# Kernel optimization log

Hardware: AMD Instinct MI355X
Metric: run time of the kernel (lower is better)

The kernel has to match this reference:

```python
import jax, jax.numpy as jnp
import numpy as np

B, T, C, K, NH, HID, L, NC = 16, 500, 512, 7, 8, 2048, 3, 2
HD = C // NH
SCALE = float(1.0 / np.sqrt(HD))


def setup_inputs() -> dict:
    key = jax.random.key(0)
    ks = jax.random.split(key, 24)
    rn = lambda k, sh, s=0.02: jax.random.normal(k, sh, jnp.float32) * s
    return {
        'x': jax.random.normal(ks[0], (B, T, C), jnp.float32),
        'dw_w': rn(ks[1], (L, NC, C, 1, K)),   # depthwise conv kernels (groups=C)
        'dw_b': rn(ks[2], (L, NC, C)),
        'pw_w': rn(ks[3], (L, NC, C, C)),       # pointwise 1x1 conv weights [out,in]
        'pw_b': rn(ks[4], (L, NC, C)),
        'cln_g': jnp.ones((L, NC, C), jnp.float32),
        'cln_b': jnp.zeros((L, NC, C), jnp.float32),
        'wq': rn(ks[5], (L, C, C)), 'bq': rn(ks[6], (L, C)),
        'wk': rn(ks[7], (L, C, C)), 'bk': rn(ks[8], (L, C)),
        'wv': rn(ks[9], (L, C, C)), 'bv': rn(ks[10], (L, C)),
        'wo': rn(ks[11], (L, C, C)), 'bo': rn(ks[12], (L, C)),
        'aln_g': jnp.ones((L, C), jnp.float32), 'aln_b': jnp.zeros((L, C), jnp.float32),
        'w1': rn(ks[13], (L, HID, C)), 'b1': rn(ks[14], (L, HID)),
        'w2': rn(ks[15], (L, C, HID)), 'b2': rn(ks[16], (L, C)),
        'fln_g': jnp.ones((L, C), jnp.float32), 'fln_b': jnp.zeros((L, C), jnp.float32),
    }


def _ln(x, g, b):
    m = x.mean(-1, keepdims=True)
    v = ((x - m) ** 2).mean(-1, keepdims=True)
    return (x - m) / jnp.sqrt(v + 1e-5) * g + b


def _conv_block(x, w, b, pw, pb, g, be):
    # x: (B, C, T). Depthwise conv (groups=C), padding K//2 keeps T.
    out = jax.lax.conv_general_dilated(
        x, w, window_strides=(1,), padding=[(K // 2, K // 2)],
        feature_group_count=C, dimension_numbers=('NCH', 'OIH', 'NCH')) + b[None, :, None]
    out = jnp.einsum('bct,oc->bot', out, pw) + pb[None, :, None]  # pointwise 1x1
    out = _ln(out.transpose(0, 2, 1), g, be).transpose(0, 2, 1)
    return out


def _attn(x, wq, bq, wk, bk, wv, bv, wo, bo):
    Bx, Tx, Cx = x.shape
    def split(h):
        return h.reshape(Bx, Tx, NH, HD).transpose(0, 2, 1, 3)  # (B,H,T,HD)
    q = split(x @ wq.T + bq)
    k = split(x @ wk.T + bk)
    v = split(x @ wv.T + bv)
    att = jnp.einsum('bhqd,bhkd->bhqk', q, k) * SCALE
    mask = jnp.tril(jnp.ones((Tx, Tx), bool))
    att = jnp.where(mask, att, -1e10)
    att = jax.nn.softmax(att, axis=-1)
    y = jnp.einsum('bhqk,bhkd->bhqd', att, v)
    y = y.transpose(0, 2, 1, 3).reshape(Bx, Tx, Cx)
    return y @ wo.T + bo


def _block(x, l, dw_w, dw_b, pw_w, pw_b, cln_g, cln_b, wq, bq, wk, bk, wv, bv,
           wo, bo, aln_g, aln_b, w1, b1, w2, b2, fln_g, fln_b):
    out = x.transpose(0, 2, 1)  # (B, C, T)
    for c in range(NC):
        out = _conv_block(out, dw_w[l, c], dw_b[l, c], pw_w[l, c], pw_b[l, c],
                          cln_g[l, c], cln_b[l, c])
    out = out.transpose(0, 2, 1)  # (B, T, C)
    out = _attn(out, wq[l], bq[l], wk[l], bk[l], wv[l], bv[l], wo[l], bo[l])
    out = _ln(out, aln_g[l], aln_b[l])
    out = _ln(jax.nn.relu(out @ w1[l].T + b1[l]) @ w2[l].T + b2[l], fln_g[l], fln_b[l])
    return out  # eval mode: dropouts are identity


def reference(x, dw_w, dw_b, pw_w, pw_b, cln_g, cln_b, wq, bq, wk, bk, wv, bv,
              wo, bo, aln_g, aln_b, w1, b1, w2, b2, fln_g, fln_b):
    outs = []
    h = x
    for l in range(L):
        h = _block(h, l, dw_w, dw_b, pw_w, pw_b, cln_g, cln_b, wq, bq, wk, bk,
                   wv, bv, wo, bo, aln_g, aln_b, w1, b1, w2, b2, fln_g, fln_b)
        outs.append(h)
    return tuple(outs)
```

## Files before the change

kernel.cpp:

```cpp
#include <hip/hip_runtime.h>
#include <hip/hip_bf16.h>

namespace {
constexpr int B = 16, T = 500, C = 512, KW = 7, NH = 8, HD = 64, HID = 2048;
constexpr int M = B * T;
constexpr float SCALE = 0.125f;
constexpr int BTC = B * T * C;
constexpr int CC = C * C;
constexpr int SEG_PW0 = 0;
constexpr int SEG_PW1 = CC;
constexpr int SEG_WQ  = 2 * CC;
constexpr int SEG_WK  = 3 * CC;
constexpr int SEG_WV  = 4 * CC;
constexpr int SEG_WO  = 5 * CC;
constexpr int SEG_W1  = 6 * CC;
constexpr int SEG_W2  = 6 * CC + HID * C;
constexpr int SEG_END = 6 * CC + 2 * HID * C;
}

typedef short s16x8 __attribute__((ext_vector_type(8)));
typedef float f32x4v __attribute__((ext_vector_type(4)));
typedef unsigned short u16x4 __attribute__((ext_vector_type(4)));

__device__ __forceinline__ unsigned int bfrne(float f) {
  unsigned int u = __float_as_uint(f);
  return (u + 0x7fffu + ((u >> 16) & 1u)) >> 16;
}
__device__ __forceinline__ unsigned int pack2(float a, float b) {
  return bfrne(a) | (bfrne(b) << 16);
}

__device__ __forceinline__ void gl_lds16(const unsigned short* g,
                                         unsigned short* l) {
  __builtin_amdgcn_global_load_lds(
      (const __attribute__((address_space(1))) void*)g,
      (__attribute__((address_space(3))) void*)l, 16, 0, 0);
}

__global__ __launch_bounds__(256) void cvtw_kernel(
    const float* __restrict__ pw0, const float* __restrict__ pw1,
    const float* __restrict__ wqp, const float* __restrict__ wkp,
    const float* __restrict__ wvp, const float* __restrict__ wop,
    const float* __restrict__ w1p, const float* __restrict__ w2p,
    unsigned short* __restrict__ dst) {
  size_t e = ((size_t)blockIdx.x * 256 + threadIdx.x) * 8;
  const float* src;
  size_t off;
  if      (e < SEG_PW1) { src = pw0; off = e - SEG_PW0; }
  else if (e < SEG_WQ)  { src = pw1; off = e - SEG_PW1; }
  else if (e < SEG_WK)  { src = wqp; off = e - SEG_WQ; }
  else if (e < SEG_WV)  { src = wkp; off = e - SEG_WK; }
  else if (e < SEG_WO)  { src = wvp; off = e - SEG_WV; }
  else if (e < SEG_W1)  { src = wop; off = e - SEG_WO; }
  else if (e < SEG_W2)  { src = w1p; off = e - SEG_W1; }
  else                  { src = w2p; off = e - SEG_W2; }
  float4 a = *(const float4*)(src + off);
  float4 b = *(const float4*)(src + off + 4);
  uint4 o;
  o.x = pack2(a.x, a.y); o.y = pack2(a.z, a.w);
  o.z = pack2(b.x, b.y); o.w = pack2(b.z, b.w);
  *(uint4*)(dst + e) = o;
}

__global__ __launch_bounds__(256) void biascat_kernel(
    const float* __restrict__ bq, const float* __restrict__ bk,
    const float* __restrict__ bv, float* __restrict__ dst) {
  int i = blockIdx.x * 256 + threadIdx.x;
  float v = (i < 512) ? bq[i] : (i < 1024 ? bk[i - 512] : bv[i - 1024]);
  dst[i] = v;
}

template <bool RELU, bool YBF>
__global__ __launch_bounds__(256) void gemm_mfma(
    const unsigned short* __restrict__ Xb,
    const unsigned short* __restrict__ Wb, const float* __restrict__ bias,
    void* __restrict__ Yv, int N, int K) {
  __shared__ unsigned short As[3][128 * 32];
  __shared__ unsigned short Bs[3][128 * 32];
  const int tid = threadIdx.x;
  const int w = tid >> 6, lane = tid & 63;
  const int quad = lane >> 4, r15 = lane & 15;

  const int gx = gridDim.x;
  const int nwg = gx * gridDim.y;
  const int orig = blockIdx.y * gx + blockIdx.x;
  const int q8 = nwg >> 3, r8 = nwg & 7;
  const int xcd = orig & 7, sidx = orig >> 3;
  const int tile =
      (xcd < r8 ? xcd * (q8 + 1) : r8 * (q8 + 1) + (xcd - r8) * q8) + sidx;
  const int n0 = (tile % gx) * 128;
  const int m0 = (tile / gx) * 128;

  const int pf = tid >> 2;
  const int cch = tid & 3;
  const int P = pf & 15;
  const int Lr = ((P & 3) << 2) | (P >> 2);
  const int lrow = (pf >> 4) * 16 + Lr;
  const int gch = cch ^ (Lr & 3);
  const size_t xa0 = (size_t)min(m0 + lrow, M - 1) * K + gch * 8;
  const size_t xa1 = (size_t)min(m0 + lrow + 64, M - 1) * K + gch * 8;
  const size_t wa0 = (size_t)(n0 + lrow) * K + gch * 8;
  const size_t wa1 = (size_t)(n0 + lrow + 64) * K + gch * 8;
  const int wbase = w * 512;

  auto issue = [&](int buf, int k0) {
    gl_lds16(Xb + xa0 + k0, &As[buf][wbase]);
    gl_lds16(Xb + xa1 + k0, &As[buf][2048 + wbase]);
    gl_lds16(Wb + wa0 + k0, &Bs[buf][wbase]);
    gl_lds16(Wb + wa1 + k0, &Bs[buf][2048 + wbase]);
  };

  const int mh = (w & 1) * 64, nh = (w >> 1) * 64;
  const int bsw = ((r15 & 3) << 2) | (r15 >> 2);
  const int chl = (quad ^ (r15 & 3)) * 8;
  const int aoff = (mh + bsw) * 32 + chl;
  const int boff = (nh + bsw) * 32 + chl;

  f32x4v acc[4][4];
#pragma unroll
  for (int i = 0; i < 4; ++i)
#pragma unroll
    for (int j = 0; j < 4; ++j) acc[i][j] = {0.f, 0.f, 0.f, 0.f};

  const int nk = K / 32;
  issue(0, 0);
  issue(1, 32);
  int cur = 0, nx2 = 2;
  for (int c = 0; c < nk; ++c) {
    if (c + 1 < nk)
      asm volatile("s_waitcnt vmcnt(4)" ::: "memory");
    else
      asm volatile("s_waitcnt vmcnt(0)" ::: "memory");
    __builtin_amdgcn_s_barrier();
    asm volatile("" ::: "memory");
    if (c + 2 < nk) issue(nx2, (c + 2) * 32);
    const unsigned short* Ac = As[cur];
    const unsigned short* Bc = Bs[cur];
    s16x8 af[4], bg[4];
#pragma unroll
    for (int im = 0; im < 4; ++im)
      af[im] = *(const s16x8*)&Ac[aoff + im * 512];
#pragma unroll
    for (int in = 0; in < 4; ++in)
      bg[in] = *(const s16x8*)&Bc[boff + in * 512];
#pragma unroll
    for (int in = 0; in < 4; ++in)
#pragma unroll
      for (int im = 0; im < 4; ++im)
        acc[im][in] = __builtin_amdgcn_mfma_f32_16x16x32_bf16(
            af[im], bg[in], acc[im][in], 0, 0, 0);
    cur = (cur == 2) ? 0 : cur + 1;
    nx2 = (nx2 == 2) ? 0 : nx2 + 1;
  }
#pragma unroll
  for (int in = 0; in < 4; ++in) {
    int col = n0 + nh + in * 16 + r15;
    float bv = bias[col];
#pragma unroll
    for (int im = 0; im < 4; ++im) {
      int rowb = m0 + mh + im * 16 + quad * 4;
#pragma unroll
      for (int r = 0; r < 4; ++r) {
        int row = rowb + r;
        if (row < M) {
          float v = acc[im][in][r] + bv;
          if (RELU) v = fmaxf(v, 0.f);
          if (YBF)
            ((unsigned short*)Yv)[(size_t)row * N + col] =
                (unsigned short)bfrne(v);
          else
            ((float*)Yv)[(size_t)row * N + col] = v;
        }
      }
    }
  }
}

__global__ __launch_bounds__(256) void dwconv_kernel(
    const float* __restrict__ X, const float* __restrict__ W,
    const float* __restrict__ bias, unsigned short* __restrict__ Y) {
  int gid = blockIdx.x * 256 + threadIdx.x;
  int b = blockIdx.y;
  int e = gid * 2;
  int t = e >> 9;
  int c = e & 511;
  float acc0 = bias[c], acc1 = bias[c + 1];
  size_t base = (size_t)b * T * C;
#pragma unroll
  for (int k = 0; k < KW; ++k) {
    int tt = t + k - 3;
    if (tt >= 0 && tt < T) {
      float2 xv = *(const float2*)&X[base + (size_t)tt * C + c];
      acc0 += xv.x * W[c * KW + k];
      acc1 += xv.y * W[(c + 1) * KW + k];
    }
  }
  *(unsigned int*)&Y[base + e] = pack2(acc0, acc1);
}

template <bool DUAL>
__global__ __launch_bounds__(256) void ln_kernel(
    const float* __restrict__ X, const float* __restrict__ g,
    const float* __restrict__ bta, float* __restrict__ Y,
    unsigned short* __restrict__ Yb) {
  int row = blockIdx.x * 4 + (threadIdx.x >> 6);
  int lane = threadIdx.x & 63;
  const float* x = X + (size_t)row * C + lane * 8;
  float4 a = *(const float4*)x;
  float4 b2 = *(const float4*)(x + 4);
  float v[8] = {a.x, a.y, a.z, a.w, b2.x, b2.y, b2.z, b2.w};
  float s = 0.f, ss = 0.f;
#pragma unroll
  for (int i = 0; i < 8; ++i) {
    s += v[i];
    ss += v[i] * v[i];
  }
#pragma unroll
  for (int off = 32; off; off >>= 1) {
    s += __shfl_xor(s, off);
    ss += __shfl_xor(ss, off);
  }
  float mean = s * (1.f / C);
  float var = ss * (1.f / C) - mean * mean;
  var = fmaxf(var, 0.f);
  float rstd = rsqrtf(var + 1e-5f);
  float4 g0 = *(const float4*)(g + lane * 8);
  float4 g1 = *(const float4*)(g + lane * 8 + 4);
  float4 be0 = *(const float4*)(bta + lane * 8);
  float4 be1 = *(const float4*)(bta + lane * 8 + 4);
  float gg[8] = {g0.x, g0.y, g0.z, g0.w, g1.x, g1.y, g1.z, g1.w};
  float bb[8] = {be0.x, be0.y, be0.z, be0.w, be1.x, be1.y, be1.z, be1.w};
  float o[8];
#pragma unroll
  for (int i = 0; i < 8; ++i) o[i] = (v[i] - mean) * rstd * gg[i] + bb[i];
  float* y = Y + (size_t)row * C + lane * 8;
  float4 w0 = {o[0], o[1], o[2], o[3]};
  float4 w1 = {o[4], o[5], o[6], o[7]};
  *(float4*)y = w0;
  *(float4*)(y + 4) = w1;
  if (DUAL) {
    uint4 ob;
    ob.x = pack2(o[0], o[1]); ob.y = pack2(o[2], o[3]);
    ob.z = pack2(o[4], o[5]); ob.w = pack2(o[6], o[7]);
    *(uint4*)(Yb + (size_t)row * C + lane * 8) = ob;
  }
}

__global__ __launch_bounds__(256) void attn_mfma_kernel(
    const unsigned short* __restrict__ QKV, unsigned short* __restrict__ Yb) {
  constexpr int QS = 3 * C;
  constexpr int LDK = 72;
  __shared__ __align__(16) unsigned short Ks[64 * LDK];
  __shared__ __align__(16) unsigned short Vt[64 * LDK];
  __shared__ __align__(16) unsigned short Ps[4][16 * LDK];
  const int tid = threadIdx.x;
  const int lane = tid & 63, w = tid >> 6;
  const int quad = lane >> 4, r15 = lane & 15;
  const int qt = blockIdx.x, hh = blockIdx.y, b = blockIdx.z;
  const int q0 = qt * 64;
  const size_t hbase = (size_t)hh * HD;

  s16x8 qa[2];
  {
    int qr = min(q0 + w * 16 + r15, T - 1);
    const unsigned short* qp = QKV + ((size_t)b * T + qr) * QS + hbase;
#pragma unroll
    for (int ks = 0; ks < 2; ++ks)
      qa[ks] = *(const s16x8*)(qp + ks * 32 + quad * 8);
  }

  f32x4v oacc[4];
  float mm[4], ll[4];
#pragma unroll
  for (int i = 0; i < 4; ++i) {
    oacc[i] = {0.f, 0.f, 0.f, 0.f};
    mm[i] = -1e30f;
    ll[i] = 0.f;
  }

  const int krow = tid >> 2, kd = (tid & 3) * 16;
  const int vk4 = (tid >> 4) * 4, vd4 = (tid & 15) * 4;

  const int kend = min(q0 + 63, T - 1);
  for (int key0 = 0; key0 <= kend; key0 += 64) {
    __syncthreads();
    {
      int key = key0 + krow;
      if (key < T) {
        const unsigned short* kp =
            QKV + ((size_t)b * T + key) * QS + C + hbase + kd;
        uint4 k0 = *(const uint4*)kp;
        uint4 k1 = *(const uint4*)(kp + 8);
        *(uint4*)&Ks[krow * LDK + kd] = k0;
        *(uint4*)&Ks[krow * LDK + kd + 8] = k1;
      } else {
        uint4 z = {0u, 0u, 0u, 0u};
        *(uint4*)&Ks[krow * LDK + kd] = z;
        *(uint4*)&Ks[krow * LDK + kd + 8] = z;
      }
    }
    {
      u16x4 va[4];
#pragma unroll
      for (int j = 0; j < 4; ++j) {
        int key = key0 + vk4 + j;
        if (key < T) {
          va[j] = *(const u16x4*)(QKV + ((size_t)b * T + key) * QS + 2 * C +
                                  hbase + vd4);
        } else {
          va[j] = (u16x4){0, 0, 0, 0};
        }
      }
#pragma unroll
      for (int i = 0; i < 4; ++i) {
        uint2 o2;
        o2.x = (unsigned int)va[0][i] | ((unsigned int)va[1][i] << 16);
        o2.y = (unsigned int)va[2][i] | ((unsigned int)va[3][i] << 16);
        *(uint2*)&Vt[(vd4 + i) * LDK + vk4] = o2;
      }
    }
    __syncthreads();

    f32x4v sa[4];
#pragma unroll
    for (int nt = 0; nt < 4; ++nt) {
      s16x8 kb0 = *(const s16x8*)&Ks[(nt * 16 + r15) * LDK + quad * 8];
      s16x8 kb1 = *(const s16x8*)&Ks[(nt * 16 + r15) * LDK + 32 + quad * 8];
      f32x4v z = {0.f, 0.f, 0.f, 0.f};
      z = __builtin_amdgcn_mfma_f32_16x16x32_bf16(qa[0], kb0, z, 0, 0, 0);
      z = __builtin_amdgcn_mfma_f32_16x16x32_bf16(qa[1], kb1, z, 0, 0, 0);
      sa[nt] = z;
    }
    const bool diag = (key0 == q0);

#pragma unroll
    for (int r = 0; r < 4; ++r) {
      int q = q0 + w * 16 + quad * 4 + r;
      float sv[4];
#pragma unroll
      for (int nt = 0; nt < 4; ++nt) {
        sv[nt] = sa[nt][r] * SCALE;
        if (diag && (key0 + nt * 16 + r15 > q)) sv[nt] = -1e30f;
      }
      float mx = fmaxf(fmaxf(sv[0], sv[1]), fmaxf(sv[2], sv[3]));
      mx = fmaxf(mx, __shfl_xor(mx, 8));
      mx = fmaxf(mx, __shfl_xor(mx, 4));
      mx = fmaxf(mx, __shfl_xor(mx, 2));
      mx = fmaxf(mx, __shfl_xor(mx, 1));
      float mnew = fmaxf(mm[r], mx);
      float alpha = __expf(mm[r] - mnew);
      float ps = 0.f;
#pragma unroll
      for (int nt = 0; nt < 4; ++nt) {
        float p = __expf(sv[nt] - mnew);
        ps += p;
        Ps[w][(quad * 4 + r) * LDK + nt * 16 + r15] =
            (unsigned short)bfrne(p);
      }
      ps += __shfl_xor(ps, 8);
      ps += __shfl_xor(ps, 4);
      ps += __shfl_xor(ps, 2);
      ps += __shfl_xor(ps, 1);
      ll[r] = ll[r] * alpha + ps;
      mm[r] = mnew;
#pragma unroll
      for (int dt = 0; dt < 4; ++dt) oacc[dt][r] *= alpha;
    }
    asm volatile("s_waitcnt lgkmcnt(0)" ::: "memory");
    __builtin_amdgcn_sched_barrier(0);

    s16x8 pa0 = *(const s16x8*)&Ps[w][r15 * LDK + quad * 8];
    s16x8 pa1 = *(const s16x8*)&Ps[w][r15 * LDK + 32 + quad * 8];
#pragma unroll
    for (int dt = 0; dt < 4; ++dt) {
      s16x8 vb0 = *(const s16x8*)&Vt[(dt * 16 + r15) * LDK + quad * 8];
      s16x8 vb1 = *(const s16x8*)&Vt[(dt * 16 + r15) * LDK + 32 + quad * 8];
      oacc[dt] =
          __builtin_amdgcn_mfma_f32_16x16x32_bf16(pa0, vb0, oacc[dt], 0, 0, 0);
      oacc[dt] =
          __builtin_amdgcn_mfma_f32_16x16x32_bf16(pa1, vb1, oacc[dt], 0, 0, 0);
    }
  }

#pragma unroll
  for (int r = 0; r < 4; ++r) {
    int q = q0 + w * 16 + quad * 4 + r;
    if (q < T) {
      float inv = 1.f / ll[r];
      unsigned short* yp = Yb + ((size_t)b * T + q) * C + hbase;
#pragma unroll
      for (int dt = 0; dt < 4; ++dt)
        yp[dt * 16 + r15] = (unsigned short)bfrne(oacc[dt][r] * inv);
    }
  }
}

extern "C" void kernel_launch(void* const* d_in, const int* in_sizes, int n_in,
                              void* d_out, int out_size, void* d_ws,
                              size_t ws_size, hipStream_t stream) {
  const float* x     = (const float*)d_in[0];
  const float* dw_w  = (const float*)d_in[1];
  const float* dw_b  = (const float*)d_in[2];
  const float* pw_w  = (const float*)d_in[3];
  const float* pw_b  = (const float*)d_in[4];
  const float* cln_g = (const float*)d_in[5];
  const float* cln_b = (const float*)d_in[6];
  const float* wq    = (const float*)d_in[7];
  const float* bq    = (const float*)d_in[8];
  const float* wk    = (const float*)d_in[9];
  const float* bk    = (const float*)d_in[10];
  const float* wv    = (const float*)d_in[11];
  const float* bv    = (const float*)d_in[12];
  const float* wo    = (const float*)d_in[13];
  const float* bo    = (const float*)d_in[14];
  const float* aln_g = (const float*)d_in[15];
  const float* aln_b = (const float*)d_in[16];
  const float* w1    = (const float*)d_in[17];
  const float* b1    = (const float*)d_in[18];
  const float* w2    = (const float*)d_in[19];
  const float* b2    = (const float*)d_in[20];
  const float* fln_g = (const float*)d_in[21];
  const float* fln_b = (const float*)d_in[22];

  float* ws = (float*)d_ws;
  float* A  = ws;
  float* Bf = ws + (size_t)BTC;
  float* R0 = ws + (size_t)2 * BTC;
  float* R1 = ws + (size_t)3 * BTC;
  float* R2 = ws + (size_t)4 * BTC;
  unsigned short* WA = (unsigned short*)(ws + (size_t)5 * BTC);
  float* out = (float*)d_out;

  unsigned short* xbf   = (unsigned short*)Bf;
  unsigned short* qkvbf = (unsigned short*)R0;
  unsigned short* fbf   = (unsigned short*)R2;
  unsigned short* hbf   = (unsigned short*)A;
  float* qkvb = A;

  dim3 blk(256);
  dim3 gemmC(C / 128, 63);
  dim3 gemmQKV(3 * C / 128, 63);
  dim3 gemmH(HID / 128, 63);
  dim3 convG(T * C / 512, B);
  dim3 attnG((T + 63) / 64, NH, B);
  int cvtwB = SEG_END / 2048;

  for (int l = 0; l < 3; ++l) {
    float* h = out + (size_t)l * BTC;
    const float* hin = (l == 0) ? x : out + (size_t)(l - 1) * BTC;
    cvtw_kernel<<<cvtwB, blk, 0, stream>>>(
        pw_w + (size_t)(2 * l) * CC, pw_w + (size_t)(2 * l + 1) * CC,
        wq + (size_t)l * CC, wk + (size_t)l * CC, wv + (size_t)l * CC,
        wo + (size_t)l * CC, w1 + (size_t)l * HID * C,
        w2 + (size_t)l * C * HID, WA);
    biascat_kernel<<<6, blk, 0, stream>>>(bq + (size_t)l * C,
                                          bk + (size_t)l * C,
                                          bv + (size_t)l * C, qkvb);
    for (int cb = 0; cb < 2; ++cb) {
      int lc = l * 2 + cb;
      const float* src = (cb == 0) ? hin : h;
      dwconv_kernel<<<convG, blk, 0, stream>>>(src, dw_w + (size_t)lc * C * KW,
                                               dw_b + (size_t)lc * C, xbf);
      gemm_mfma<false, false><<<gemmC, blk, 0, stream>>>(
          xbf, WA + (cb ? SEG_PW1 : SEG_PW0), pw_b + (size_t)lc * C, R0, C, C);
      if (cb == 0)
        ln_kernel<false><<<M / 4, blk, 0, stream>>>(
            R0, cln_g + (size_t)lc * C, cln_b + (size_t)lc * C, h, nullptr);
      else
        ln_kernel<true><<<M / 4, blk, 0, stream>>>(
            R0, cln_g + (size_t)lc * C, cln_b + (size_t)lc * C, h, xbf);
    }
    gemm_mfma<false, true><<<gemmQKV, blk, 0, stream>>>(
        xbf, WA + SEG_WQ, qkvb, qkvbf, 3 * C, C);
    attn_mfma_kernel<<<attnG, blk, 0, stream>>>(qkvbf, xbf);
    gemm_mfma<false, false><<<gemmC, blk, 0, stream>>>(
        xbf, WA + SEG_WO, bo + (size_t)l * C, R1, C, C);
    ln_kernel<true><<<M / 4, blk, 0, stream>>>(
        R1, aln_g + (size_t)l * C, aln_b + (size_t)l * C, h, fbf);
    gemm_mfma<true, true><<<gemmH, blk, 0, stream>>>(
        fbf, WA + SEG_W1, b1 + (size_t)l * HID, hbf, HID, C);
    gemm_mfma<false, false><<<gemmC, blk, 0, stream>>>(
        hbf, WA + SEG_W2, b2 + (size_t)l * C, R0, C, HID);
    ln_kernel<false><<<M / 4, blk, 0, stream>>>(
        R0, fln_g + (size_t)l * C, fln_b + (size_t)l * C, h, nullptr);
  }
}
```

Baseline: 1.098 ms.

## Run GEMM tiles with 8 waves per block, each owning a 32x64 sub-tile

The 128x128 bf16 MFMA GEMM now launches 512 threads (8 waves) instead of 256. Each wave computes a 32x64 sub-tile with half the accumulators, and each thread issues one global-to-LDS load per operand per k-step instead of two. The swizzled row permutation is simplified to a plain XOR channel swizzle, and the compiler fence becomes a sched_barrier. The goal is more waves in flight to hide latency and lower register pressure, at the cost of more LDS fragment reads per MFMA and possible new bank conflicts.

```diff
diff --git a/kernel.cpp b/kernel.cpp
--- a/kernel.cpp
+++ b/kernel.cpp
@@ -71,7 +71,7 @@
 }
 
 template <bool RELU, bool YBF>
-__global__ __launch_bounds__(256) void gemm_mfma(
+__global__ __launch_bounds__(512) void gemm_mfma(
     const unsigned short* __restrict__ Xb,
     const unsigned short* __restrict__ Wb, const float* __restrict__ bias,
     void* __restrict__ Yv, int N, int K) {
@@ -91,73 +91,62 @@
   const int n0 = (tile % gx) * 128;
   const int m0 = (tile / gx) * 128;
 
-  const int pf = tid >> 2;
-  const int cch = tid & 3;
-  const int P = pf & 15;
-  const int Lr = ((P & 3) << 2) | (P >> 2);
-  const int lrow = (pf >> 4) * 16 + Lr;
-  const int gch = cch ^ (Lr & 3);
-  const size_t xa0 = (size_t)min(m0 + lrow, M - 1) * K + gch * 8;
-  const size_t xa1 = (size_t)min(m0 + lrow + 64, M - 1) * K + gch * 8;
-  const size_t wa0 = (size_t)(n0 + lrow) * K + gch * 8;
-  const size_t wa1 = (size_t)(n0 + lrow + 64) * K + gch * 8;
-  const int wbase = w * 512;
+  const int srow = lane >> 2;
+  const int gch = ((lane & 3) ^ (srow & 3)) * 8;
+  const size_t xsrc = (size_t)min(m0 + w * 16 + srow, M - 1) * K + gch;
+  const size_t wsrc = (size_t)(n0 + w * 16 + srow) * K + gch;
 
   auto issue = [&](int buf, int k0) {
-    gl_lds16(Xb + xa0 + k0, &As[buf][wbase]);
-    gl_lds16(Xb + xa1 + k0, &As[buf][2048 + wbase]);
-    gl_lds16(Wb + wa0 + k0, &Bs[buf][wbase]);
-    gl_lds16(Wb + wa1 + k0, &Bs[buf][2048 + wbase]);
+    gl_lds16(Xb + xsrc + k0, &As[buf][w * 512]);
+    gl_lds16(Wb + wsrc + k0, &Bs[buf][w * 512]);
   };
 
-  const int mh = (w & 1) * 64, nh = (w >> 1) * 64;
-  const int bsw = ((r15 & 3) << 2) | (r15 >> 2);
-  const int chl = (quad ^ (r15 & 3)) * 8;
-  const int aoff = (mh + bsw) * 32 + chl;
-  const int boff = (nh + bsw) * 32 + chl;
-
-  f32x4v acc[4][4];
-#pragma unroll
-  for (int i = 0; i < 4; ++i)
+  const int wm = w >> 1, wn = w & 1;
+  const int mh = wm * 32, nh = wn * 64;
+  const int c0 = (quad ^ (r15 & 3)) * 8;
+
+  f32x4v acc[2][4];
+#pragma unroll
+  for (int i = 0; i < 2; ++i)
 #pragma unroll
     for (int j = 0; j < 4; ++j) acc[i][j] = {0.f, 0.f, 0.f, 0.f};
 
   const int nk = K / 32;
   issue(0, 0);
   issue(1, 32);
-  int cur = 0, nx2 = 2;
+  int cur = 0, nxt = 2;
   for (int c = 0; c < nk; ++c) {
     if (c + 1 < nk)
-      asm volatile("s_waitcnt vmcnt(4)" ::: "memory");
+      asm volatile("s_waitcnt vmcnt(2)" ::: "memory");
     else
       asm volatile("s_waitcnt vmcnt(0)" ::: "memory");
     __builtin_amdgcn_s_barrier();
-    asm volatile("" ::: "memory");
-    if (c + 2 < nk) issue(nx2, (c + 2) * 32);
+    __builtin_amdgcn_sched_barrier(0);
+    if (c + 2 < nk) issue(nxt, (c + 2) * 32);
     const unsigned short* Ac = As[cur];
     const unsigned short* Bc = Bs[cur];
-    s16x8 af[4], bg[4];
-#pragma unroll
-    for (int im = 0; im < 4; ++im)
-      af[im] = *(const s16x8*)&Ac[aoff + im * 512];
+    s16x8 af[2], bg[4];
+#pragma unroll
+    for (int im = 0; im < 2; ++im)
+      af[im] = *(const s16x8*)&Ac[(mh + im * 16 + r15) * 32 + c0];
 #pragma unroll
     for (int in = 0; in < 4; ++in)
-      bg[in] = *(const s16x8*)&Bc[boff + in * 512];
+      bg[in] = *(const s16x8*)&Bc[(nh + in * 16 + r15) * 32 + c0];
 #pragma unroll
     for (int in = 0; in < 4; ++in)
 #pragma unroll
-      for (int im = 0; im < 4; ++im)
+      for (int im = 0; im < 2; ++im)
         acc[im][in] = __builtin_amdgcn_mfma_f32_16x16x32_bf16(
             af[im], bg[in], acc[im][in], 0, 0, 0);
     cur = (cur == 2) ? 0 : cur + 1;
-    nx2 = (nx2 == 2) ? 0 : nx2 + 1;
+    nxt = (nxt == 2) ? 0 : nxt + 1;
   }
 #pragma unroll
   for (int in = 0; in < 4; ++in) {
     int col = n0 + nh + in * 16 + r15;
     float bv = bias[col];
 #pragma unroll
-    for (int im = 0; im < 4; ++im) {
+    for (int im = 0; im < 2; ++im) {
       int rowb = m0 + mh + im * 16 + quad * 4;
 #pragma unroll
       for (int r = 0; r < 4; ++r) {
@@ -438,6 +427,7 @@
   float* qkvb = A;
 
   dim3 blk(256);
+  dim3 blkG(512);
   dim3 gemmC(C / 128, 63);
   dim3 gemmQKV(3 * C / 128, 63);
   dim3 gemmH(HID / 128, 63);
@@ -461,7 +451,7 @@
       const float* src = (cb == 0) ? hin : h;
       dwconv_kernel<<<convG, blk, 0, stream>>>(src, dw_w + (size_t)lc * C * KW,
                                                dw_b + (size_t)lc * C, xbf);
-      gemm_mfma<false, false><<<gemmC, blk, 0, stream>>>(
+      gemm_mfma<false, false><<<gemmC, blkG, 0, stream>>>(
           xbf, WA + (cb ? SEG_PW1 : SEG_PW0), pw_b + (size_t)lc * C, R0, C, C);
       if (cb == 0)
         ln_kernel<false><<<M / 4, blk, 0, stream>>>(
@@ -470,16 +460,16 @@
         ln_kernel<true><<<M / 4, blk, 0, stream>>>(
             R0, cln_g + (size_t)lc * C, cln_b + (size_t)lc * C, h, xbf);
     }
-    gemm_mfma<false, true><<<gemmQKV, blk, 0, stream>>>(
+    gemm_mfma<false, true><<<gemmQKV, blkG, 0, stream>>>(
         xbf, WA + SEG_WQ, qkvb, qkvbf, 3 * C, C);
     attn_mfma_kernel<<<attnG, blk, 0, stream>>>(qkvbf, xbf);
-    gemm_mfma<false, false><<<gemmC, blk, 0, stream>>>(
+    gemm_mfma<false, false><<<gemmC, blkG, 0, stream>>>(
         xbf, WA + SEG_WO, bo + (size_t)l * C, R1, C, C);
     ln_kernel<true><<<M / 4, blk, 0, stream>>>(
         R1, aln_g + (size_t)l * C, aln_b + (size_t)l * C, h, fbf);
-    gemm_mfma<true, true><<<gemmH, blk, 0, stream>>>(
+    gemm_mfma<true, true><<<gemmH, blkG, 0, stream>>>(
         fbf, WA + SEG_W1, b1 + (size_t)l * HID, hbf, HID, C);
-    gemm_mfma<false, false><<<gemmC, blk, 0, stream>>>(
+    gemm_mfma<false, false><<<gemmC, blkG, 0, stream>>>(
         hbf, WA + SEG_W2, b2 + (size_t)l * C, R0, C, HID);
     ln_kernel<false><<<M / 4, blk, 0, stream>>>(
         R0, fln_g + (size_t)l * C, fln_b + (size_t)l * C, h, nullptr);
```

Result: faster. 1.046 ms (-4.7%).
